# Kernel tuning notes

Measured on AMD Instinct MI355X. Metric: run time of the kernel, lower is better.

The kernel has to match this reference:

```python
import jax, jax.numpy as jnp
import numpy as np
from jax import lax

B, N, C = 16, 16384, 90      # batch, anchors, classes
K = 100                      # per-class pre-NMS top-k
MAX_DET = 100                # final detections per image
IOU_THR = 0.5
SCORE_THR = 0.05


def setup_inputs() -> dict:
    key = jax.random.key(0)
    k1, k2, k3, k4 = jax.random.split(key, 4)
    box_encodings = jax.random.normal(k1, (B, N, 4), dtype=jnp.float32) * 0.5
    class_logits = jax.random.normal(k2, (B, N, C), dtype=jnp.float32) * 2.0 - 3.0
    # anchors as [ymin,xmin,ymax,xmax] in normalized coords
    centers = jax.random.uniform(k3, (N, 2), dtype=jnp.float32)             # (cy,cx)
    sizes = jax.random.uniform(k4, (N, 2), dtype=jnp.float32, minval=0.05, maxval=0.3)
    anchors = jnp.concatenate([centers - sizes / 2, centers + sizes / 2], axis=-1)
    return {"box_encodings": box_encodings, "class_logits": class_logits, "anchors": anchors}


def decode_boxes(enc, anchors):
    ymin, xmin, ymax, xmax = [anchors[:, i] for i in range(4)]
    ha, wa = ymax - ymin, xmax - xmin
    cya, cxa = (ymin + ymax) / 2, (xmin + xmax) / 2
    ty, tx, th, tw = enc[..., 0] / 10.0, enc[..., 1] / 10.0, enc[..., 2] / 5.0, enc[..., 3] / 5.0
    cy = ty * ha + cya
    cx = tx * wa + cxa
    h = jnp.exp(th) * ha
    w = jnp.exp(tw) * wa
    boxes = jnp.stack([cy - h / 2, cx - w / 2, cy + h / 2, cx + w / 2], axis=-1)
    return jnp.clip(boxes, 0.0, 1.0)  # [..., N, 4]


def pairwise_iou(b):  # b: [K,4]
    area = jnp.maximum(b[:, 2] - b[:, 0], 0) * jnp.maximum(b[:, 3] - b[:, 1], 0)
    iy = jnp.maximum(jnp.minimum(b[:, None, 2], b[None, :, 2]) - jnp.maximum(b[:, None, 0], b[None, :, 0]), 0)
    ix = jnp.maximum(jnp.minimum(b[:, None, 3], b[None, :, 3]) - jnp.maximum(b[:, None, 1], b[None, :, 1]), 0)
    inter = iy * ix
    union = area[:, None] + area[None, :] - inter
    return inter / jnp.maximum(union, 1e-8)


def nms_one_class(boxes, scores_c):  # boxes [N,4], scores_c [N]
    vals, idx = lax.top_k(scores_c, K)           # sorted descending
    bk = boxes[idx]                               # [K,4]
    iou = pairwise_iou(bk)                        # [K,K]
    def step(keep, i):
        supp = jnp.any(keep & (iou[i] >= IOU_THR))
        ki = (vals[i] > SCORE_THR) & (~supp)
        return keep.at[i].set(ki), None
    keep, _ = lax.scan(step, jnp.zeros((K,), bool), jnp.arange(K))
    return bk, vals * keep                        # suppressed -> score 0


def postprocess_one(boxes, scores):  # boxes [N,4], scores [N,C]
    bx_ck, sc_ck = jax.vmap(nms_one_class, in_axes=(None, 1))(boxes, scores)  # [C,K,4],[C,K]
    cls_ck = jnp.broadcast_to(jnp.arange(C, dtype=jnp.float32)[:, None], (C, K))
    sc_f = sc_ck.reshape(-1)
    fsc, fidx = lax.top_k(sc_f, MAX_DET)
    fbx = bx_ck.reshape(-1, 4)[fidx]
    fcl = cls_ck.reshape(-1)[fidx]
    return jnp.concatenate([fbx, fcl[:, None], fsc[:, None]], axis=-1)  # [MAX_DET, 6]


def reference(box_encodings, class_logits, anchors):
    boxes = decode_boxes(box_encodings, anchors)       # [B,N,4]
    scores = jax.nn.sigmoid(class_logits)              # [B,N,C]
    combined = jax.vmap(postprocess_one)(boxes, scores)  # [B,MAX_DET,6] = boxes|class|score
    return combined
```

## Files before the change

kernel.cpp:

```cpp
#include <hip/hip_runtime.h>
#include <stdint.h>
#include <math.h>

#define B_ 16
#define NN 16384
#define C_ 90
#define KSEL 100
#define MAXD 100
#define MFLAT (C_ * KSEL)
#define NPAIR 128


__device__ __forceinline__ uint32_t fkey(float f) {
  uint32_t u = __float_as_uint(f);
  return (u & 0x80000000u) ? ~u : (u | 0x80000000u);
}
__device__ __forceinline__ float keyinv(uint32_t k) {
  uint32_t u = (k & 0x80000000u) ? (k & 0x7FFFFFFFu) : ~k;
  return __uint_as_float(u);
}

__device__ __forceinline__ uint32_t blockSum512(uint32_t v, uint32_t* red, uint32_t* s_total) {
  int tid = threadIdx.x;
#pragma unroll
  for (int o = 32; o > 0; o >>= 1) v += __shfl_down(v, o, 64);
  if ((tid & 63) == 0) red[tid >> 6] = v;
  __syncthreads();
  if (tid == 0) {
    uint32_t s = 0;
#pragma unroll
    for (int i = 0; i < 8; ++i) s += red[i];
    *s_total = s;
  }
  __syncthreads();
  return *s_total;
}

__device__ __forceinline__ uint32_t blockSum256(uint32_t v, uint32_t* red, uint32_t* s_total) {
  int tid = threadIdx.x;
#pragma unroll
  for (int o = 32; o > 0; o >>= 1) v += __shfl_down(v, o, 64);
  if ((tid & 63) == 0) red[tid >> 6] = v;
  __syncthreads();
  if (tid == 0) *s_total = red[0] + red[1] + red[2] + red[3];
  __syncthreads();
  return *s_total;
}

__global__ __launch_bounds__(256) void transpose_sig_kernel(const float* __restrict__ logits,
                                                            uint32_t* __restrict__ keysT) {
  __shared__ uint32_t tile[128 * 91];
  int b = blockIdx.y;
  int n0 = blockIdx.x * 128;
  const float4* src4 = reinterpret_cast<const float4*>(logits + ((size_t)b * NN + n0) * C_);
  for (int p = threadIdx.x; p < 2880; p += 256) {
    float4 v = src4[p];
    int e = p * 4;
    float vv[4] = {v.x, v.y, v.z, v.w};
#pragma unroll
    for (int j = 0; j < 4; ++j) {
      int ee = e + j;
      float s = 1.0f / (1.0f + expf(-vv[j]));
      tile[(ee / C_) * 91 + (ee % C_)] = fkey(s);
    }
  }
  __syncthreads();
  uint32_t* dstb = keysT + (size_t)b * C_ * NN + n0;
  for (int q = threadIdx.x; q < C_ * 32; q += 256) {
    int c = q >> 5, g = q & 31;
    int nn2 = g * 4;
    uint4 o;
    o.x = tile[nn2 * 91 + c];
    o.y = tile[(nn2 + 1) * 91 + c];
    o.z = tile[(nn2 + 2) * 91 + c];
    o.w = tile[(nn2 + 3) * 91 + c];
    reinterpret_cast<uint4*>(dstb + (size_t)c * NN)[g] = o;
  }
}

template <int TR>
__global__ __launch_bounds__(512, 4) void select_kernel(
    const uint32_t* __restrict__ keysT,
    const float* __restrict__ logits,
    unsigned long long* __restrict__ candPairs,
    uint32_t* __restrict__ candCount) {
  __shared__ uint32_t hist[2048];
  __shared__ uint32_t sc[512];
  __shared__ uint32_t ws8[64];
  __shared__ int s_bsel;
  __shared__ uint32_t s_Sincl, s_Sexcl;
  __shared__ uint32_t red[8];
  __shared__ uint32_t s_total;
  __shared__ uint32_t s_cnt;

  const int c = blockIdx.x, b = blockIdx.y;
  const int tid = threadIdx.x;

  uint32_t key[32];
  if (TR) {
    const uint4* src4 = reinterpret_cast<const uint4*>(keysT + ((size_t)b * C_ + c) * NN);
#pragma unroll
    for (int q = 0; q < 8; ++q) {
      uint4 kv = src4[q * 512 + tid];
      key[4 * q + 0] = kv.x; key[4 * q + 1] = kv.y;
      key[4 * q + 2] = kv.z; key[4 * q + 3] = kv.w;
    }
  } else {
    const float* src = logits + (size_t)b * NN * C_ + c;
#pragma unroll
    for (int q = 0; q < 8; ++q) {
#pragma unroll
      for (int j = 0; j < 4; ++j) {
        int idx = (q * 512 + tid) * 4 + j;
        float x = src[(size_t)idx * C_];
        key[4 * q + j] = fkey(1.0f / (1.0f + expf(-x)));
      }
    }
  }

  uint32_t cutHi = 0;
  uint32_t m_above = 0;
  uint32_t cut30 = 0;
  int found = 0;
  int tiepath = 0;
  uint32_t V30 = 0, Texact = NN - 1;

  for (int lvl = 0; lvl < 3; ++lvl) {
    const int shiftLo = (lvl == 0) ? 19 : (lvl == 1) ? 8 : 0;
    const int shiftHi = (lvl == 0) ? 30 : (lvl == 1) ? 19 : 8;
    const uint32_t mask = (lvl == 2) ? 0xFFu : 0x7FFu;
    const int nbits = (lvl == 2) ? 8 : 11;

    for (int i = tid; i < 2048; i += 512) hist[i] = 0;
    __syncthreads();
#pragma unroll
    for (int q = 0; q < 32; ++q) {
      uint32_t k30 = key[q] & 0x3FFFFFFFu;
      if ((k30 >> shiftHi) == cutHi)
        atomicAdd(&hist[(k30 >> shiftLo) & mask], 1u);
    }
    __syncthreads();

    const uint32_t need = 100u - m_above;

    uint32_t h0 = hist[4 * tid], h1 = hist[4 * tid + 1];
    uint32_t h2 = hist[4 * tid + 2], h3 = hist[4 * tid + 3];
    sc[tid] = h0 + h1 + h2 + h3;
    if (tid == 0) s_bsel = -1;
    __syncthreads();
    if (tid < 64) {
      uint32_t w = 0;
      int base = tid * 8;
#pragma unroll
      for (int i = 0; i < 8; ++i) w += sc[base + i];
#pragma unroll
      for (int off = 1; off < 64; off <<= 1) {
        uint32_t v = __shfl_down(w, off, 64);
        if (tid + off < 64) w += v;
      }
      ws8[tid] = w;
    }
    __syncthreads();
    {
      int g = tid >> 3;
      uint32_t above = (g < 63) ? ws8[g + 1] : 0u;
      for (int j = (g << 3) + 7; j > tid; --j) above += sc[j];
      uint32_t run = above;
      int best = -1;
      uint32_t bi = 0, be = 0;
      uint32_t hh[4] = {h0, h1, h2, h3};
#pragma unroll
      for (int p = 3; p >= 0; --p) {
        uint32_t h = hh[p];
        run += h;
        if (best < 0 && run >= need) { best = 4 * tid + p; bi = run; be = run - h; }
      }
      if (best >= 0) atomicMax(&s_bsel, best);
      __syncthreads();
      if (best >= 0 && best == s_bsel) { s_Sincl = bi; s_Sexcl = be; }
    }
    __syncthreads();

    uint32_t bsel = (uint32_t)s_bsel;
    uint32_t Sincl = s_Sincl, Sexcl = s_Sexcl;
    cutHi = (cutHi << nbits) | bsel;
    if (m_above + Sincl <= (uint32_t)NPAIR) {
      cut30 = cutHi << shiftLo;
      found = 1;
      break;
    }
    m_above += Sexcl;
  }

  if (!found) {
    tiepath = 1;
    V30 = cutHi;
    uint32_t r = 100u - m_above;
    uint32_t lo2 = 0, hi2 = NN - 1;
    while (lo2 < hi2) {
      uint32_t mid2 = lo2 + ((hi2 - lo2) >> 1);
      uint32_t cnt = 0;
#pragma unroll
      for (int q = 0; q < 8; ++q)
#pragma unroll
        for (int j = 0; j < 4; ++j) {
          uint32_t idx = (uint32_t)((q * 512 + tid) * 4 + j);
          cnt += ((key[4 * q + j] & 0x3FFFFFFFu) == V30 && idx <= mid2) ? 1u : 0u;
        }
      uint32_t tot = blockSum512(cnt, red, &s_total);
      if (tot >= r) hi2 = mid2; else lo2 = mid2 + 1;
    }
    Texact = lo2;
  }

  if (tid == 0) s_cnt = 0;
  __syncthreads();
  unsigned long long* outp = candPairs + (size_t)(b * C_ + c) * NPAIR;
#pragma unroll
  for (int q = 0; q < 8; ++q) {
#pragma unroll
    for (int j = 0; j < 4; ++j) {
      uint32_t kf = key[4 * q + j];
      uint32_t k30 = kf & 0x3FFFFFFFu;
      uint32_t idx = (uint32_t)((q * 512 + tid) * 4 + j);
      bool take = tiepath ? (k30 > V30 || (k30 == V30 && idx <= Texact))
                          : (k30 >= cut30);
      if (take) {
        uint32_t p = atomicAdd(&s_cnt, 1u);
        if (p < (uint32_t)NPAIR)
          outp[p] = ((unsigned long long)kf << 32) | (unsigned long long)(~idx);
      }
    }
  }
  __syncthreads();
  if (tid == 0) candCount[b * C_ + c] = (s_cnt > (uint32_t)NPAIR) ? (uint32_t)NPAIR : s_cnt;
}

__global__ __launch_bounds__(128, 4) void sort_nms_kernel(
    const unsigned long long* __restrict__ candPairs,
    const uint32_t* __restrict__ candCount,
    const float* __restrict__ enc,
    const float* __restrict__ anchors,
    float* __restrict__ candBox,
    float* __restrict__ candScore) {
  __shared__ unsigned long long ck[NPAIR];
  __shared__ float s_vals[KSEL];
  __shared__ float s_boxv[KSEL][5];
  __shared__ float s_area[KSEL];
  __shared__ uint32_t smask[KSEL][4];
  __shared__ unsigned long long s_keepw[2];

  const int c = blockIdx.x, b = blockIdx.y;
  const int tid = threadIdx.x;
  const int bc = b * C_ + c;

  uint32_t cnt = candCount[bc];
  ck[tid] = (tid < (int)cnt) ? candPairs[(size_t)bc * NPAIR + tid] : 0ull;
  __syncthreads();

  for (int kk = 2; kk <= 128; kk <<= 1) {
    for (int j = kk >> 1; j > 0; j >>= 1) {
      int ixj = tid ^ j;
      if (ixj > tid) {
        unsigned long long a = ck[tid], bb2 = ck[ixj];
        if ((a < bb2) == ((tid & kk) == 0)) { ck[tid] = bb2; ck[ixj] = a; }
      }
      __syncthreads();
    }
  }

  if (tid < KSEL) {
    unsigned long long keyv = ck[tid];
    uint32_t hk = (uint32_t)(keyv >> 32);
    int n = (int)(~(uint32_t)(keyv & 0xFFFFFFFFull)) & (NN - 1);
    s_vals[tid] = keyinv(hk);
    float4 e = reinterpret_cast<const float4*>(enc)[(size_t)b * NN + n];
    float4 a = reinterpret_cast<const float4*>(anchors)[n];
    float ha = a.z - a.x, wa = a.w - a.y;
    float cya = (a.x + a.z) * 0.5f, cxa = (a.y + a.w) * 0.5f;
    float cy = (e.x / 10.0f) * ha + cya;
    float cx = (e.y / 10.0f) * wa + cxa;
    float h = expf(e.z / 5.0f) * ha;
    float w = expf(e.w / 5.0f) * wa;
    float y1 = fminf(fmaxf(cy - h * 0.5f, 0.0f), 1.0f);
    float x1 = fminf(fmaxf(cx - w * 0.5f, 0.0f), 1.0f);
    float y2 = fminf(fmaxf(cy + h * 0.5f, 0.0f), 1.0f);
    float x2 = fminf(fmaxf(cx + w * 0.5f, 0.0f), 1.0f);
    s_boxv[tid][0] = y1; s_boxv[tid][1] = x1; s_boxv[tid][2] = y2; s_boxv[tid][3] = x2;
    s_area[tid] = fmaxf(y2 - y1, 0.0f) * fmaxf(x2 - x1, 0.0f);
    smask[tid][0] = 0; smask[tid][1] = 0; smask[tid][2] = 0; smask[tid][3] = 0;
  }
  __syncthreads();

  for (int p = tid; p < (KSEL * (KSEL - 1)) / 2; p += 128) {
    int j = (int)((1.0f + sqrtf(1.0f + 8.0f * (float)p)) * 0.5f);
    while (j * (j - 1) / 2 > p) --j;
    while ((j + 1) * j / 2 <= p) ++j;
    int i = p - j * (j - 1) / 2;
    float iy1 = s_boxv[i][0], ix1 = s_boxv[i][1], iy2 = s_boxv[i][2], ix2 = s_boxv[i][3];
    float jy1 = s_boxv[j][0], jx1 = s_boxv[j][1], jy2 = s_boxv[j][2], jx2 = s_boxv[j][3];
    float ta = fmaxf(fminf(iy2, jy2) - fmaxf(iy1, jy1), 0.0f) *
               fmaxf(fminf(ix2, jx2) - fmaxf(ix1, jx1), 0.0f);
    float un = fmaxf(s_area[i] + s_area[j] - ta, 1e-8f);
    if (ta / un >= 0.5f) atomicOr(&smask[i][j >> 5], 1u << (j & 31));
  }
  __syncthreads();

  if (tid < 64) {
    int L = tid;
    unsigned long long r0 = (unsigned long long)smask[L][0] |
                            ((unsigned long long)smask[L][1] << 32);
    unsigned long long r1 = (unsigned long long)smask[L][2] |
                            ((unsigned long long)smask[L][3] << 32);
    unsigned long long r2 = 0, r3 = 0;
    if (L < KSEL - 64) {
      r2 = (unsigned long long)smask[L + 64][0] | ((unsigned long long)smask[L + 64][1] << 32);
      r3 = (unsigned long long)smask[L + 64][2] | ((unsigned long long)smask[L + 64][3] << 32);
    }
    unsigned long long vm0 = __ballot(s_vals[L] > 0.05f);
    unsigned long long vm1 = __ballot((L + 64 < KSEL) ? (s_vals[L + 64] > 0.05f) : false);
    unsigned long long supp0 = 0, supp1 = 0, k0 = 0, k1 = 0;
    for (int j = 0; j < KSEL; ++j) {
      unsigned long long rl, rh;
      bool pass;
      if (j < 64) {
        rl = __shfl(r0, j); rh = __shfl(r1, j);
        pass = ((vm0 >> j) & 1ull) && !((supp0 >> j) & 1ull);
      } else {
        rl = __shfl(r2, j - 64); rh = __shfl(r3, j - 64);
        pass = ((vm1 >> (j - 64)) & 1ull) && !((supp1 >> (j - 64)) & 1ull);
      }
      if (pass) {
        supp0 |= rl; supp1 |= rh;
        if (j < 64) k0 |= 1ull << j; else k1 |= 1ull << (j - 64);
      }
    }
    if (tid == 0) { s_keepw[0] = k0; s_keepw[1] = k1; }
  }
  __syncthreads();

  if (tid < KSEL) {
    bool kept = (tid < 64) ? ((s_keepw[0] >> tid) & 1ull)
                           : ((s_keepw[1] >> (tid - 64)) & 1ull);
    size_t base = (size_t)bc * KSEL + tid;
    candScore[base] = kept ? s_vals[tid] : 0.0f;
    float* cb = candBox + base * 4;
    cb[0] = s_boxv[tid][0]; cb[1] = s_boxv[tid][1];
    cb[2] = s_boxv[tid][2]; cb[3] = s_boxv[tid][3];
  }
}

#define FSLOT 36
__global__ __launch_bounds__(256, 4) void final_topk_kernel(
    const float* __restrict__ candScore,
    const float* __restrict__ candBox,
    float* __restrict__ out) {
  __shared__ uint32_t red[4];
  __shared__ uint32_t s_total;
  __shared__ uint32_t s_cnt;
  __shared__ unsigned long long ck[128];

  int b = blockIdx.x, tid = threadIdx.x;
  const float* src = candScore + (size_t)b * MFLAT;

  uint32_t key[FSLOT];
#pragma unroll
  for (int q = 0; q < FSLOT; ++q) {
    int idx = q * 256 + tid;
    key[q] = (idx < MFLAT) ? fkey(src[idx]) : 0u;
  }

  uint32_t lo = 0u, hi = 0xFFFFFFFFu;
  while (lo < hi) {
    uint32_t mid = lo + ((hi - lo) >> 1);
    uint32_t cnt = 0;
#pragma unroll
    for (int q = 0; q < FSLOT; ++q) cnt += (key[q] > mid) ? 1u : 0u;
    uint32_t tot = blockSum256(cnt, red, &s_total);
    if (tot >= (uint32_t)MAXD) lo = mid + 1; else hi = mid;
  }
  uint32_t V = lo;

  uint32_t cm = 0, ce = 0;
#pragma unroll
  for (int q = 0; q < FSLOT; ++q) {
    cm += (key[q] > V) ? 1u : 0u;
    ce += (key[q] == V) ? 1u : 0u;
  }
  uint32_t m = blockSum256(cm, red, &s_total);
  uint32_t t = blockSum256(ce, red, &s_total);
  uint32_t r = (uint32_t)MAXD - m;
  uint32_t T = (uint32_t)(MFLAT - 1);
  if (t != r) {
    uint32_t lo2 = 0, hi2 = (uint32_t)(MFLAT - 1);
    while (lo2 < hi2) {
      uint32_t mid2 = lo2 + ((hi2 - lo2) >> 1);
      uint32_t cnt = 0;
#pragma unroll
      for (int q = 0; q < FSLOT; ++q) {
        uint32_t idx = (uint32_t)(q * 256 + tid);
        cnt += (key[q] == V && idx <= mid2) ? 1u : 0u;
      }
      uint32_t tot = blockSum256(cnt, red, &s_total);
      if (tot >= r) hi2 = mid2; else lo2 = mid2 + 1;
    }
    T = lo2;
  }

  if (tid == 0) s_cnt = 0;
  __syncthreads();
#pragma unroll
  for (int q = 0; q < FSLOT; ++q) {
    uint32_t k = key[q];
    uint32_t idx = (uint32_t)(q * 256 + tid);
    if (k > V || (k == V && idx <= T)) {
      uint32_t p = atomicAdd(&s_cnt, 1u);
      if (p < 128u)
        ck[p] = ((unsigned long long)k << 32) | (unsigned long long)(~idx);
    }
  }
  __syncthreads();
  if (tid >= MAXD && tid < 128) ck[tid] = 0ull;
  __syncthreads();
  for (int kk = 2; kk <= 128; kk <<= 1) {
    for (int j = kk >> 1; j > 0; j >>= 1) {
      if (tid < 128) {
        int ixj = tid ^ j;
        if (ixj > tid) {
          unsigned long long a = ck[tid], bb = ck[ixj];
          if ((a < bb) == ((tid & kk) == 0)) { ck[tid] = bb; ck[ixj] = a; }
        }
      }
      __syncthreads();
    }
  }

  if (tid < MAXD) {
    unsigned long long keyv = ck[tid];
    int f = (int)(~(uint32_t)(keyv & 0xFFFFFFFFull));
    int c = f / KSEL;
    float sc = keyinv((uint32_t)(keyv >> 32));
    const float* cb = candBox + ((size_t)b * MFLAT + f) * 4;
    float* o = out + ((size_t)b * MAXD + tid) * 6;
    o[0] = cb[0]; o[1] = cb[1]; o[2] = cb[2]; o[3] = cb[3];
    o[4] = (float)c; o[5] = sc;
  }
}

extern "C" void kernel_launch(void* const* d_in, const int* in_sizes, int n_in,
                              void* d_out, int out_size, void* d_ws, size_t ws_size,
                              hipStream_t stream) {
  const float* enc = (const float*)d_in[0];
  const float* logits = (const float*)d_in[1];
  const float* anchors = (const float*)d_in[2];
  float* out = (float*)d_out;
  char* ws = (char*)d_ws;

  size_t off = 0;
  float* candBox = (float*)(ws + off);   off += (size_t)B_ * C_ * KSEL * 4 * sizeof(float);
  float* candScore = (float*)(ws + off); off += (size_t)B_ * C_ * KSEL * sizeof(float);
  unsigned long long* candPairs = (unsigned long long*)(ws + off);
  off += (size_t)B_ * C_ * NPAIR * sizeof(unsigned long long);
  uint32_t* candCount = (uint32_t*)(ws + off); off += (size_t)B_ * C_ * sizeof(uint32_t);
  uint32_t* keysT = (uint32_t*)(ws + off);
  size_t needT = off + (size_t)B_ * C_ * NN * sizeof(uint32_t);
  int transposed = (ws_size >= needT) ? 1 : 0;

  if (transposed) {
    transpose_sig_kernel<<<dim3(NN / 128, B_), 256, 0, stream>>>(logits, keysT);
    select_kernel<1><<<dim3(C_, B_), 512, 0, stream>>>(keysT, logits, candPairs, candCount);
  } else {
    select_kernel<0><<<dim3(C_, B_), 512, 0, stream>>>(keysT, logits, candPairs, candCount);
  }

  sort_nms_kernel<<<dim3(C_, B_), 128, 0, stream>>>(candPairs, candCount, enc, anchors,
                                                    candBox, candScore);

  final_topk_kernel<<<B_, 256, 0, stream>>>(candScore, candBox, out);
}
```

Baseline: 166.5 us.

## Select top-k on 16-bit logit keys and recompute sigmoid only for candidates

The transpose kernel now stores the upper 16 bits of the order-preserving key of the raw logit instead of a 32-bit sigmoid key. This halves the transposed buffer and drops the per-element exp from the transpose pass. The top-k selection builds one 2048-bin histogram from the 16-bit keys, refines with a 32-bin pass or an index tie-break when needed, and emits packed 32-bit (key16, index) candidates. The sort/NMS kernel reloads the original logits for the candidates to rebuild exact sigmoid keys. It relies on sigmoid being monotonic and on the 16-bit truncation keeping at most 128 candidates in the selected set; tie handling at 16-bit resolution may pick different elements than full precision.

Result: faster. 151.4 us (-9.1%).

```diff
diff --git a/kernel.cpp b/kernel.cpp
--- a/kernel.cpp
+++ b/kernel.cpp
@@ -47,8 +47,8 @@
   return *s_total;
 }
 
-__global__ __launch_bounds__(256) void transpose_sig_kernel(const float* __restrict__ logits,
-                                                            uint32_t* __restrict__ keysT) {
+__global__ __launch_bounds__(256) void transpose_key16_kernel(const float* __restrict__ logits,
+                                                              uint16_t* __restrict__ keys16T) {
   __shared__ uint32_t tile[128 * 91];
   int b = blockIdx.y;
   int n0 = blockIdx.x * 128;
@@ -60,29 +60,28 @@
 #pragma unroll
     for (int j = 0; j < 4; ++j) {
       int ee = e + j;
-      float s = 1.0f / (1.0f + expf(-vv[j]));
-      tile[(ee / C_) * 91 + (ee % C_)] = fkey(s);
-    }
-  }
-  __syncthreads();
-  uint32_t* dstb = keysT + (size_t)b * C_ * NN + n0;
-  for (int q = threadIdx.x; q < C_ * 32; q += 256) {
-    int c = q >> 5, g = q & 31;
-    int nn2 = g * 4;
+      tile[(ee / C_) * 91 + (ee % C_)] = fkey(vv[j]);
+    }
+  }
+  __syncthreads();
+  uint16_t* dstb = keys16T + (size_t)b * C_ * NN + n0;
+  for (int q = threadIdx.x; q < C_ * 16; q += 256) {
+    int c = q >> 4, g = q & 15;
+    int nn2 = g * 8;
     uint4 o;
-    o.x = tile[nn2 * 91 + c];
-    o.y = tile[(nn2 + 1) * 91 + c];
-    o.z = tile[(nn2 + 2) * 91 + c];
-    o.w = tile[(nn2 + 3) * 91 + c];
+    o.x = (tile[(nn2 + 0) * 91 + c] >> 16) | (tile[(nn2 + 1) * 91 + c] & 0xFFFF0000u);
+    o.y = (tile[(nn2 + 2) * 91 + c] >> 16) | (tile[(nn2 + 3) * 91 + c] & 0xFFFF0000u);
+    o.z = (tile[(nn2 + 4) * 91 + c] >> 16) | (tile[(nn2 + 5) * 91 + c] & 0xFFFF0000u);
+    o.w = (tile[(nn2 + 6) * 91 + c] >> 16) | (tile[(nn2 + 7) * 91 + c] & 0xFFFF0000u);
     reinterpret_cast<uint4*>(dstb + (size_t)c * NN)[g] = o;
   }
 }
 
 template <int TR>
 __global__ __launch_bounds__(512, 4) void select_kernel(
-    const uint32_t* __restrict__ keysT,
+    const uint16_t* __restrict__ keys16T,
     const float* __restrict__ logits,
-    unsigned long long* __restrict__ candPairs,
+    uint32_t* __restrict__ candPacked,
     uint32_t* __restrict__ candCount) {
   __shared__ uint32_t hist[2048];
   __shared__ uint32_t sc[512];
@@ -96,53 +95,44 @@
   const int c = blockIdx.x, b = blockIdx.y;
   const int tid = threadIdx.x;
 
-  uint32_t key[32];
+  uint32_t keyw[16];
   if (TR) {
-    const uint4* src4 = reinterpret_cast<const uint4*>(keysT + ((size_t)b * C_ + c) * NN);
-#pragma unroll
-    for (int q = 0; q < 8; ++q) {
+    const uint4* src4 = reinterpret_cast<const uint4*>(keys16T + ((size_t)b * C_ + c) * NN);
+#pragma unroll
+    for (int q = 0; q < 4; ++q) {
       uint4 kv = src4[q * 512 + tid];
-      key[4 * q + 0] = kv.x; key[4 * q + 1] = kv.y;
-      key[4 * q + 2] = kv.z; key[4 * q + 3] = kv.w;
+      keyw[4 * q + 0] = kv.x; keyw[4 * q + 1] = kv.y;
+      keyw[4 * q + 2] = kv.z; keyw[4 * q + 3] = kv.w;
     }
   } else {
     const float* src = logits + (size_t)b * NN * C_ + c;
 #pragma unroll
-    for (int q = 0; q < 8; ++q) {
-#pragma unroll
-      for (int j = 0; j < 4; ++j) {
-        int idx = (q * 512 + tid) * 4 + j;
-        float x = src[(size_t)idx * C_];
-        key[4 * q + j] = fkey(1.0f / (1.0f + expf(-x)));
-      }
-    }
-  }
-
-  uint32_t cutHi = 0;
+    for (int m = 0; m < 16; ++m) {
+      uint32_t i0 = (uint32_t)((((m >> 2) * 512 + tid) * 8) + ((m & 3) * 2));
+      uint32_t klo = fkey(src[(size_t)i0 * C_]) >> 16;
+      uint32_t khi = fkey(src[(size_t)(i0 + 1) * C_]) >> 16;
+      keyw[m] = klo | (khi << 16);
+    }
+  }
+
+  reinterpret_cast<uint4*>(hist)[tid] = make_uint4(0u, 0u, 0u, 0u);
+  __syncthreads();
+#pragma unroll
+  for (int m = 0; m < 16; ++m) {
+    uint32_t w = keyw[m];
+    atomicAdd(&hist[(w & 0xFFFFu) >> 5], 1u);
+    atomicAdd(&hist[w >> 21], 1u);
+  }
+  __syncthreads();
+
   uint32_t m_above = 0;
-  uint32_t cut30 = 0;
+  uint32_t need = 100u;
+  uint32_t cut16 = 0;
   int found = 0;
   int tiepath = 0;
-  uint32_t V30 = 0, Texact = NN - 1;
-
-  for (int lvl = 0; lvl < 3; ++lvl) {
-    const int shiftLo = (lvl == 0) ? 19 : (lvl == 1) ? 8 : 0;
-    const int shiftHi = (lvl == 0) ? 30 : (lvl == 1) ? 19 : 8;
-    const uint32_t mask = (lvl == 2) ? 0xFFu : 0x7FFu;
-    const int nbits = (lvl == 2) ? 8 : 11;
-
-    for (int i = tid; i < 2048; i += 512) hist[i] = 0;
-    __syncthreads();
-#pragma unroll
-    for (int q = 0; q < 32; ++q) {
-      uint32_t k30 = key[q] & 0x3FFFFFFFu;
-      if ((k30 >> shiftHi) == cutHi)
-        atomicAdd(&hist[(k30 >> shiftLo) & mask], 1u);
-    }
-    __syncthreads();
-
-    const uint32_t need = 100u - m_above;
-
+  uint32_t V16 = 0, Texact = NN - 1;
+
+  {
     uint32_t h0 = hist[4 * tid], h1 = hist[4 * tid + 1];
     uint32_t h2 = hist[4 * tid + 2], h3 = hist[4 * tid + 3];
     sc[tid] = h0 + h1 + h2 + h3;
@@ -183,53 +173,76 @@
 
     uint32_t bsel = (uint32_t)s_bsel;
     uint32_t Sincl = s_Sincl, Sexcl = s_Sexcl;
-    cutHi = (cutHi << nbits) | bsel;
-    if (m_above + Sincl <= (uint32_t)NPAIR) {
-      cut30 = cutHi << shiftLo;
+    if (Sincl <= (uint32_t)NPAIR) {
+      cut16 = bsel << 5;
       found = 1;
-      break;
-    }
-    m_above += Sexcl;
-  }
-
-  if (!found) {
-    tiepath = 1;
-    V30 = cutHi;
-    uint32_t r = 100u - m_above;
-    uint32_t lo2 = 0, hi2 = NN - 1;
-    while (lo2 < hi2) {
-      uint32_t mid2 = lo2 + ((hi2 - lo2) >> 1);
-      uint32_t cnt = 0;
-#pragma unroll
-      for (int q = 0; q < 8; ++q)
-#pragma unroll
-        for (int j = 0; j < 4; ++j) {
-          uint32_t idx = (uint32_t)((q * 512 + tid) * 4 + j);
-          cnt += ((key[4 * q + j] & 0x3FFFFFFFu) == V30 && idx <= mid2) ? 1u : 0u;
+    } else {
+      m_above = Sexcl;
+      need = 100u - m_above;
+      __syncthreads();
+      if (tid < 8) reinterpret_cast<uint4*>(hist)[tid] = make_uint4(0u, 0u, 0u, 0u);
+      __syncthreads();
+#pragma unroll
+      for (int m = 0; m < 16; ++m) {
+        uint32_t w = keyw[m];
+        uint32_t klo = w & 0xFFFFu, khi = w >> 16;
+        if ((klo >> 5) == bsel) atomicAdd(&hist[klo & 31u], 1u);
+        if ((khi >> 5) == bsel) atomicAdd(&hist[khi & 31u], 1u);
+      }
+      __syncthreads();
+      uint32_t run = 0;
+      int b1 = -1;
+      uint32_t Si = 0, Se = 0;
+      for (int p = 31; p >= 0; --p) {
+        uint32_t h = hist[p];
+        run += h;
+        if (b1 < 0 && run >= need) { b1 = p; Si = run; Se = run - h; }
+      }
+      uint32_t cutv = (bsel << 5) | (uint32_t)b1;
+      if (m_above + Si <= (uint32_t)NPAIR) {
+        cut16 = cutv;
+        found = 1;
+      } else {
+        tiepath = 1;
+        V16 = cutv;
+        m_above += Se;
+        uint32_t r = 100u - m_above;
+        uint32_t lo2 = 0, hi2 = NN - 1;
+        while (lo2 < hi2) {
+          uint32_t mid2 = lo2 + ((hi2 - lo2) >> 1);
+          uint32_t cnt = 0;
+#pragma unroll
+          for (int m = 0; m < 16; ++m) {
+            uint32_t w = keyw[m];
+            uint32_t i0 = (uint32_t)((((m >> 2) * 512 + tid) * 8) + ((m & 3) * 2));
+            cnt += ((w & 0xFFFFu) == V16 && i0 <= mid2) ? 1u : 0u;
+            cnt += ((w >> 16) == V16 && (i0 + 1) <= mid2) ? 1u : 0u;
+          }
+          uint32_t tot = blockSum512(cnt, red, &s_total);
+          if (tot >= r) hi2 = mid2; else lo2 = mid2 + 1;
         }
-      uint32_t tot = blockSum512(cnt, red, &s_total);
-      if (tot >= r) hi2 = mid2; else lo2 = mid2 + 1;
-    }
-    Texact = lo2;
+        Texact = lo2;
+      }
+    }
   }
 
   if (tid == 0) s_cnt = 0;
   __syncthreads();
-  unsigned long long* outp = candPairs + (size_t)(b * C_ + c) * NPAIR;
-#pragma unroll
-  for (int q = 0; q < 8; ++q) {
-#pragma unroll
-    for (int j = 0; j < 4; ++j) {
-      uint32_t kf = key[4 * q + j];
-      uint32_t k30 = kf & 0x3FFFFFFFu;
-      uint32_t idx = (uint32_t)((q * 512 + tid) * 4 + j);
-      bool take = tiepath ? (k30 > V30 || (k30 == V30 && idx <= Texact))
-                          : (k30 >= cut30);
-      if (take) {
-        uint32_t p = atomicAdd(&s_cnt, 1u);
-        if (p < (uint32_t)NPAIR)
-          outp[p] = ((unsigned long long)kf << 32) | (unsigned long long)(~idx);
-      }
+  uint32_t* outp = candPacked + (size_t)(b * C_ + c) * NPAIR;
+#pragma unroll
+  for (int m = 0; m < 16; ++m) {
+    uint32_t w = keyw[m];
+    uint32_t i0 = (uint32_t)((((m >> 2) * 512 + tid) * 8) + ((m & 3) * 2));
+    uint32_t klo = w & 0xFFFFu, khi = w >> 16;
+    bool t0 = tiepath ? (klo > V16 || (klo == V16 && i0 <= Texact)) : (klo >= cut16);
+    bool t1 = tiepath ? (khi > V16 || (khi == V16 && (i0 + 1) <= Texact)) : (khi >= cut16);
+    if (t0) {
+      uint32_t p = atomicAdd(&s_cnt, 1u);
+      if (p < (uint32_t)NPAIR) outp[p] = (klo << 16) | i0;
+    }
+    if (t1) {
+      uint32_t p = atomicAdd(&s_cnt, 1u);
+      if (p < (uint32_t)NPAIR) outp[p] = (khi << 16) | (i0 + 1);
     }
   }
   __syncthreads();
@@ -237,8 +250,9 @@
 }
 
 __global__ __launch_bounds__(128, 4) void sort_nms_kernel(
-    const unsigned long long* __restrict__ candPairs,
+    const uint32_t* __restrict__ candPacked,
     const uint32_t* __restrict__ candCount,
+    const float* __restrict__ logits,
     const float* __restrict__ enc,
     const float* __restrict__ anchors,
     float* __restrict__ candBox,
@@ -255,7 +269,15 @@
   const int bc = b * C_ + c;
 
   uint32_t cnt = candCount[bc];
-  ck[tid] = (tid < (int)cnt) ? candPairs[(size_t)bc * NPAIR + tid] : 0ull;
+  unsigned long long ckv = 0ull;
+  if (tid < (int)cnt) {
+    uint32_t v = candPacked[(size_t)bc * NPAIR + tid];
+    int n = (int)(v & 0x3FFFu);
+    float x = logits[((size_t)b * NN + n) * C_ + c];
+    float s = 1.0f / (1.0f + expf(-x));
+    ckv = ((unsigned long long)fkey(s) << 32) | (unsigned long long)(~(uint32_t)n);
+  }
+  ck[tid] = ckv;
   __syncthreads();
 
   for (int kk = 2; kk <= 128; kk <<= 1) {
@@ -459,22 +481,23 @@
   size_t off = 0;
   float* candBox = (float*)(ws + off);   off += (size_t)B_ * C_ * KSEL * 4 * sizeof(float);
   float* candScore = (float*)(ws + off); off += (size_t)B_ * C_ * KSEL * sizeof(float);
-  unsigned long long* candPairs = (unsigned long long*)(ws + off);
-  off += (size_t)B_ * C_ * NPAIR * sizeof(unsigned long long);
+  uint32_t* candPacked = (uint32_t*)(ws + off);
+  off += (size_t)B_ * C_ * NPAIR * sizeof(uint32_t);
   uint32_t* candCount = (uint32_t*)(ws + off); off += (size_t)B_ * C_ * sizeof(uint32_t);
-  uint32_t* keysT = (uint32_t*)(ws + off);
-  size_t needT = off + (size_t)B_ * C_ * NN * sizeof(uint32_t);
+  off = (off + 255) & ~(size_t)255;
+  uint16_t* keys16T = (uint16_t*)(ws + off);
+  size_t needT = off + (size_t)B_ * C_ * NN * sizeof(uint16_t);
   int transposed = (ws_size >= needT) ? 1 : 0;
 
   if (transposed) {
-    transpose_sig_kernel<<<dim3(NN / 128, B_), 256, 0, stream>>>(logits, keysT);
-    select_kernel<1><<<dim3(C_, B_), 512, 0, stream>>>(keysT, logits, candPairs, candCount);
+    transpose_key16_kernel<<<dim3(NN / 128, B_), 256, 0, stream>>>(logits, keys16T);
+    select_kernel<1><<<dim3(C_, B_), 512, 0, stream>>>(keys16T, logits, candPacked, candCount);
   } else {
-    select_kernel<0><<<dim3(C_, B_), 512, 0, stream>>>(keysT, logits, candPairs, candCount);
-  }
-
-  sort_nms_kernel<<<dim3(C_, B_), 128, 0, stream>>>(candPairs, candCount, enc, anchors,
-                                                    candBox, candScore);
+    select_kernel<0><<<dim3(C_, B_), 512, 0, stream>>>(keys16T, logits, candPacked, candCount);
+  }
+
+  sort_nms_kernel<<<dim3(C_, B_), 128, 0, stream>>>(candPacked, candCount, logits,
+                                                    enc, anchors, candBox, candScore);
 
   final_topk_kernel<<<B_, 256, 0, stream>>>(candScore, candBox, out);
 }
```
